# Performance work log

Measured on AMD Instinct MI355X. Metric: run time of the kernel, lower is better.

Reference implementation:

```python
import jax, jax.numpy as jnp
import numpy as np

N_NODES, N_EDGES = 50000, 200000
DN, DE, DG = 256, 256, 128

def setup_inputs() -> dict:
    key = jax.random.key(0)
    ks = jax.random.split(key, 8)
    s = lambda d: 1.0 / np.sqrt(d)
    return {
        "nodes": jax.random.normal(ks[0], (N_NODES, DN), jnp.float32),
        "edges": jax.random.normal(ks[1], (N_EDGES, DE), jnp.float32),
        "globals_": jax.random.normal(ks[2], (DG,), jnp.float32),
        "senders": jax.random.randint(ks[3], (N_EDGES,), 0, N_NODES, jnp.int32),
        "receivers": jax.random.randint(ks[4], (N_EDGES,), 0, N_NODES, jnp.int32),
        "We": jax.random.normal(ks[5], (DE + 2 * DN + DG, DE), jnp.float32) * s(DE + 2 * DN + DG),
        "be": jnp.zeros((DE,), jnp.float32),
        "Wn": jax.random.normal(ks[6], (DE + DN + DG, DN), jnp.float32) * s(DE + DN + DG),
        "bn": jnp.zeros((DN,), jnp.float32),
        "Wg": jax.random.normal(ks[7], (DE + DN + DG, DG), jnp.float32) * s(DE + DN + DG),
        "bg": jnp.zeros((DG,), jnp.float32),
    }

def reference(nodes, edges, globals_, senders, receivers, We, be, Wn, bn, Wg, bg):
    E, N = edges.shape[0], nodes.shape[0]
    # --- edge processor: phi_e([e, v_s, v_r, u]) ---
    edge_in = jnp.concatenate(
        [edges, nodes[senders], nodes[receivers],
         jnp.broadcast_to(globals_, (E, globals_.shape[0]))], axis=-1)  # [E, 896]
    new_edges = jax.nn.relu(edge_in @ We + be)  # [E, DE]
    # --- node processor: phi_v([sum_incoming_e, v, u]) ---
    agg_e = jax.ops.segment_sum(new_edges, receivers, num_segments=N)  # [N, DE]
    node_in = jnp.concatenate(
        [agg_e, nodes, jnp.broadcast_to(globals_, (N, globals_.shape[0]))], axis=-1)
    new_nodes = jax.nn.relu(node_in @ Wn + bn)  # [N, DN]
    # --- global processor: phi_u([sum_e, sum_v, u]) ---
    global_in = jnp.concatenate(
        [new_edges.sum(axis=0), new_nodes.sum(axis=0), globals_], axis=-1)
    new_globals = jax.nn.relu(global_in @ Wg + bg)  # [DG]
    return new_edges, new_nodes, new_globals
```

## Files before the change

kernel.cpp:

```cpp
#include <hip/hip_runtime.h>

#define E_CNT 200000
#define N_CNT 50000

typedef __attribute__((ext_vector_type(8))) unsigned short ushort8;
typedef __attribute__((ext_vector_type(4))) float f32x4;
typedef __bf16 bf16x8 __attribute__((ext_vector_type(8)));

static __device__ __forceinline__ unsigned short f2bf(float f) {
  unsigned int u = __builtin_bit_cast(unsigned int, f);
  u += 0x7FFFu + ((u >> 16) & 1u);
  return (unsigned short)(u >> 16);
}

typedef const __attribute__((address_space(1))) void gvoid;
typedef __attribute__((address_space(3))) void lvoid;
static __device__ __forceinline__ void gload_lds16(const void* g, void* l) {
  __builtin_amdgcn_global_load_lds((gvoid*)g, (lvoid*)l, 16, 0, 0);
}

__global__ void prep_w(const float* __restrict__ W, unsigned short* __restrict__ Bp, int KC) {
  int idx = blockIdx.x * blockDim.x + threadIdx.x;
  int total = KC * 16 * 64;
  if (idx >= total) return;
  int lane = idx & 63;
  int t = idx >> 6;
  int F = t & 15;
  int kc = t >> 4;
  int col = F * 16 + (lane & 15);
  int kb = kc * 32 + (lane >> 4) * 8;
  ushort8 v;
#pragma unroll
  for (int j = 0; j < 8; ++j) v[j] = f2bf(W[(size_t)(kb + j) * 256 + col]);
  *reinterpret_cast<ushort8*>(Bp + (size_t)idx * 8) = v;
}

template <int NSTEPS, bool EDGE>
__global__ __launch_bounds__(512, 4) void gemm_mlp(
    const float* __restrict__ in0, const float* __restrict__ nodes,
    const float* __restrict__ gl, const int* __restrict__ senders,
    const int* __restrict__ receivers, const unsigned short* __restrict__ Bp,
    const float* __restrict__ bias, float* __restrict__ out,
    float* __restrict__ agg, int M) {
  __shared__ float ldsA[2][64 * 64];

  const int tid = threadIdx.x;
  const int lane = tid & 63;
  const int wave = tid >> 6;
  const int wm = wave >> 2;
  const int wn = wave & 3;
  const int q = lane >> 4;
  const int lr = lane & 15;
  const int row0 = blockIdx.x * 64;

  int rl[2];
  const float* bp[2][4];
#pragma unroll
  for (int i = 0; i < 2; ++i) {
    rl[i] = wave * 8 + i * 4 + q;
    int e = row0 + rl[i];
    if (e > M - 1) e = M - 1;
    if (EDGE) {
      bp[i][0] = in0 + (size_t)e * 256;
      bp[i][1] = nodes + (size_t)senders[e] * 256;
      bp[i][2] = nodes + (size_t)receivers[e] * 256;
      bp[i][3] = gl;
    } else {
      bp[i][0] = in0 + (size_t)e * 256;
      bp[i][1] = nodes + (size_t)e * 256;
      bp[i][2] = gl;
      bp[i][3] = gl;
    }
  }

  f32x4 acc[2][4] = {};

#pragma unroll
  for (int i = 0; i < 2; ++i) {
    const float* src = bp[i][0] + ((lr ^ (rl[i] & 15)) << 2);
    gload_lds16(src, &ldsA[0][(wave * 8 + i * 4) * 64]);
  }
  __syncthreads();

#pragma unroll
  for (int ks = 0; ks < NSTEPS; ++ks) {
    const int buf = ks & 1;

    bf16x8 bfr[2][4];
#pragma unroll
    for (int kk = 0; kk < 2; ++kk) {
      const int kc32 = ks * 2 + kk;
#pragma unroll
      for (int fn = 0; fn < 4; ++fn) {
        const int F = wn * 4 + fn;
        bfr[kk][fn] = __builtin_bit_cast(
            bf16x8, *reinterpret_cast<const ushort8*>(
                        Bp + ((size_t)(kc32 * 16 + F) * 64 + lane) * 8));
      }
    }

    if (ks + 1 < NSTEPS) {
      const int seg = (ks + 1) >> 2;
      const int off = ((ks + 1) & 3) * 64;
#pragma unroll
      for (int i = 0; i < 2; ++i) {
        const float* src = bp[i][seg] + off + ((lr ^ (rl[i] & 15)) << 2);
        gload_lds16(src, &ldsA[buf ^ 1][(wave * 8 + i * 4) * 64]);
      }
    }
    __builtin_amdgcn_sched_barrier(0);

#pragma unroll
    for (int kk = 0; kk < 2; ++kk) {
      bf16x8 a[2];
#pragma unroll
      for (int fm = 0; fm < 2; ++fm) {
        const int r = wm * 32 + fm * 16 + lr;
        const int x = r & 15;
        const int u0 = kk * 8 + q * 2;
        f32x4 lo = *reinterpret_cast<const f32x4*>(
            &ldsA[buf][r * 64 + ((u0 ^ x) << 2)]);
        f32x4 hi = *reinterpret_cast<const f32x4*>(
            &ldsA[buf][r * 64 + (((u0 + 1) ^ x) << 2)]);
        bf16x8 av;
        av[0] = (__bf16)lo[0]; av[1] = (__bf16)lo[1];
        av[2] = (__bf16)lo[2]; av[3] = (__bf16)lo[3];
        av[4] = (__bf16)hi[0]; av[5] = (__bf16)hi[1];
        av[6] = (__bf16)hi[2]; av[7] = (__bf16)hi[3];
        a[fm] = av;
      }
#pragma unroll
      for (int fm = 0; fm < 2; ++fm)
#pragma unroll
        for (int fn = 0; fn < 4; ++fn)
          acc[fm][fn] = __builtin_amdgcn_mfma_f32_16x16x32_bf16(
              a[fm], bfr[kk][fn], acc[fm][fn], 0, 0, 0);
    }
    __syncthreads();
  }

  float bcol[4];
#pragma unroll
  for (int fn = 0; fn < 4; ++fn) bcol[fn] = bias[wn * 64 + fn * 16 + lr];
#pragma unroll
  for (int fm = 0; fm < 2; ++fm) {
    int rb = row0 + wm * 32 + fm * 16 + q * 4;
#pragma unroll
    for (int i = 0; i < 4; ++i) {
      int gr = rb + i;
      if (gr < M) {
        int rcv = 0;
        if (EDGE) rcv = receivers[gr];
#pragma unroll
        for (int fn = 0; fn < 4; ++fn) {
          int col = wn * 64 + fn * 16 + lr;
          float v = fmaxf(acc[fm][fn][i] + bcol[fn], 0.0f);
          if (EDGE) {
            __builtin_nontemporal_store(v, &out[(size_t)gr * 256 + col]);
            atomicAdd(agg + (size_t)rcv * 256 + col, v);
          } else {
            out[(size_t)gr * 256 + col] = v;
          }
        }
      }
    }
  }
}

__global__ void colsum_p1(const float* __restrict__ in, float* __restrict__ part, int rows) {
  const int c4 = threadIdx.x & 63;
  const int rg = threadIdx.x >> 6;
  f32x4 s = {0.f, 0.f, 0.f, 0.f};
  for (int r = blockIdx.x * 4 + rg; r < rows; r += 256)
    s += *reinterpret_cast<const f32x4*>(in + (size_t)r * 256 + c4 * 4);
  __shared__ f32x4 red[256];
  red[threadIdx.x] = s;
  __syncthreads();
  if (rg == 0) {
    f32x4 r = red[c4] + red[64 + c4] + red[128 + c4] + red[192 + c4];
    *reinterpret_cast<f32x4*>(part + (size_t)blockIdx.x * 256 + c4 * 4) = r;
  }
}

__global__ void colsum_p2(const float* __restrict__ part, float* __restrict__ out) {
  const int c = threadIdx.x;
  float s = 0.f;
  for (int p = 0; p < 64; ++p) s += part[(size_t)p * 256 + c];
  out[c] = s;
}

__global__ void global_mlp(const float* __restrict__ esum, const float* __restrict__ nsum,
                           const float* __restrict__ gl, const float* __restrict__ Wg,
                           const float* __restrict__ bg, float* __restrict__ out2) {
  __shared__ float red[512];
  int g = threadIdx.x & 127;
  int kg = threadIdx.x >> 7;
  float acc = 0.f;
  for (int k = kg; k < 640; k += 4) {
    float x = (k < 256) ? esum[k] : (k < 512 ? nsum[k - 256] : gl[k - 512]);
    acc += x * Wg[(size_t)k * 128 + g];
  }
  red[threadIdx.x] = acc;
  __syncthreads();
  if (kg == 0) {
    float r = red[g] + red[128 + g] + red[256 + g] + red[384 + g] + bg[g];
    out2[g] = fmaxf(r, 0.f);
  }
}

extern "C" void kernel_launch(void* const* d_in, const int* in_sizes, int n_in,
                              void* d_out, int out_size, void* d_ws, size_t ws_size,
                              hipStream_t stream) {
  const float* nodes = (const float*)d_in[0];
  const float* edges = (const float*)d_in[1];
  const float* gl = (const float*)d_in[2];
  const int* senders = (const int*)d_in[3];
  const int* receivers = (const int*)d_in[4];
  const float* We = (const float*)d_in[5];
  const float* be = (const float*)d_in[6];
  const float* Wn = (const float*)d_in[7];
  const float* bn = (const float*)d_in[8];
  const float* Wg = (const float*)d_in[9];
  const float* bg = (const float*)d_in[10];

  float* out0 = (float*)d_out;
  float* out1 = out0 + (size_t)E_CNT * 256;
  float* out2 = out1 + (size_t)N_CNT * 256;

  char* ws = (char*)d_ws;
  size_t o = 0;
  float* agg = (float*)(ws + o);                   o += (size_t)N_CNT * 256 * 4;
  float* esum = (float*)(ws + o);                  o += 1024;
  float* nsum = (float*)(ws + o);                  o += 1024;
  float* partE = (float*)(ws + o);                 o += 64 * 256 * 4;
  float* partN = (float*)(ws + o);                 o += 64 * 256 * 4;
  unsigned short* BpE = (unsigned short*)(ws + o); o += 458752;
  unsigned short* BpN = (unsigned short*)(ws + o); o += 327680;

  hipMemsetAsync(agg, 0, (size_t)N_CNT * 256 * 4, stream);

  prep_w<<<112, 256, 0, stream>>>(We, BpE, 28);
  prep_w<<<80, 256, 0, stream>>>(Wn, BpN, 20);

  gemm_mlp<14, true><<<E_CNT / 64, 512, 0, stream>>>(
      edges, nodes, gl, senders, receivers, BpE, be, out0, agg, E_CNT);

  colsum_p1<<<64, 256, 0, stream>>>(agg, partE, N_CNT);
  colsum_p2<<<1, 256, 0, stream>>>(partE, esum);

  gemm_mlp<10, false><<<(N_CNT + 63) / 64, 512, 0, stream>>>(
      agg, nodes, gl, nullptr, nullptr, BpN, bn, out1, nullptr, N_CNT);

  colsum_p1<<<64, 256, 0, stream>>>(out1, partN, N_CNT);
  colsum_p2<<<1, 256, 0, stream>>>(partN, nsum);

  global_mlp<<<1, 512, 0, stream>>>(esum, nsum, gl, Wg, bg, out2);
}
```

Before: 529.5 us.

## Pre-convert node features to bf16 and load A fragments directly into registers

Adds a pass that converts node features and globals to bf16 once, so the gathered sender/receiver rows read half the bytes. The GEMM drops the LDS double-buffered global_load_lds staging and syncthreads, loading A fragments directly from global memory into registers for each 32-wide K chunk. Column-sum partial count is doubled. This trades away the prefetch/overlap pipeline and its coalesced staging for fewer bytes and no barriers, and adds an extra conversion kernel and workspace.

```diff
diff --git a/kernel.cpp b/kernel.cpp
--- a/kernel.cpp
+++ b/kernel.cpp
@@ -11,12 +11,6 @@
   unsigned int u = __builtin_bit_cast(unsigned int, f);
   u += 0x7FFFu + ((u >> 16) & 1u);
   return (unsigned short)(u >> 16);
-}
-
-typedef const __attribute__((address_space(1))) void gvoid;
-typedef __attribute__((address_space(3))) void lvoid;
-static __device__ __forceinline__ void gload_lds16(const void* g, void* l) {
-  __builtin_amdgcn_global_load_lds((gvoid*)g, (lvoid*)l, 16, 0, 0);
 }
 
 __global__ void prep_w(const float* __restrict__ W, unsigned short* __restrict__ Bp, int KC) {
@@ -35,15 +29,28 @@
   *reinterpret_cast<ushort8*>(Bp + (size_t)idx * 8) = v;
 }
 
+__global__ void cvt_bf16(const float* __restrict__ in, unsigned short* __restrict__ outp,
+                         int n8) {
+  int i = blockIdx.x * blockDim.x + threadIdx.x;
+  if (i >= n8) return;
+  f32x4 a = *reinterpret_cast<const f32x4*>(in + (size_t)i * 8);
+  f32x4 b = *reinterpret_cast<const f32x4*>(in + (size_t)i * 8 + 4);
+  ushort8 v;
+#pragma unroll
+  for (int j = 0; j < 4; ++j) {
+    v[j] = f2bf(a[j]);
+    v[4 + j] = f2bf(b[j]);
+  }
+  *reinterpret_cast<ushort8*>(outp + (size_t)i * 8) = v;
+}
+
 template <int NSTEPS, bool EDGE>
 __global__ __launch_bounds__(512, 4) void gemm_mlp(
-    const float* __restrict__ in0, const float* __restrict__ nodes,
-    const float* __restrict__ gl, const int* __restrict__ senders,
+    const float* __restrict__ in0, const unsigned short* __restrict__ nbf,
+    const unsigned short* __restrict__ glb, const int* __restrict__ senders,
     const int* __restrict__ receivers, const unsigned short* __restrict__ Bp,
     const float* __restrict__ bias, float* __restrict__ out,
     float* __restrict__ agg, int M) {
-  __shared__ float ldsA[2][64 * 64];
-
   const int tid = threadIdx.x;
   const int lane = tid & 63;
   const int wave = tid >> 6;
@@ -51,92 +58,71 @@
   const int wn = wave & 3;
   const int q = lane >> 4;
   const int lr = lane & 15;
-  const int row0 = blockIdx.x * 64;
-
-  int rl[2];
-  const float* bp[2][4];
-#pragma unroll
-  for (int i = 0; i < 2; ++i) {
-    rl[i] = wave * 8 + i * 4 + q;
-    int e = row0 + rl[i];
-    if (e > M - 1) e = M - 1;
+  const int rowW = blockIdx.x * 64 + wm * 32;
+
+  const float* p0[2];
+  const unsigned short* p1[2];
+  const unsigned short* p2[2];
+#pragma unroll
+  for (int fm = 0; fm < 2; ++fm) {
+    int r = rowW + fm * 16 + lr;
+    if (r > M - 1) r = M - 1;
+    p0[fm] = in0 + (size_t)r * 256;
     if (EDGE) {
-      bp[i][0] = in0 + (size_t)e * 256;
-      bp[i][1] = nodes + (size_t)senders[e] * 256;
-      bp[i][2] = nodes + (size_t)receivers[e] * 256;
-      bp[i][3] = gl;
+      p1[fm] = nbf + (size_t)senders[r] * 256;
+      p2[fm] = nbf + (size_t)receivers[r] * 256;
     } else {
-      bp[i][0] = in0 + (size_t)e * 256;
-      bp[i][1] = nodes + (size_t)e * 256;
-      bp[i][2] = gl;
-      bp[i][3] = gl;
+      p1[fm] = nbf + (size_t)r * 256;
+      p2[fm] = nbf;
     }
   }
 
   f32x4 acc[2][4] = {};
 
 #pragma unroll
-  for (int i = 0; i < 2; ++i) {
-    const float* src = bp[i][0] + ((lr ^ (rl[i] & 15)) << 2);
-    gload_lds16(src, &ldsA[0][(wave * 8 + i * 4) * 64]);
-  }
-  __syncthreads();
-
-#pragma unroll
-  for (int ks = 0; ks < NSTEPS; ++ks) {
-    const int buf = ks & 1;
-
-    bf16x8 bfr[2][4];
-#pragma unroll
-    for (int kk = 0; kk < 2; ++kk) {
-      const int kc32 = ks * 2 + kk;
-#pragma unroll
-      for (int fn = 0; fn < 4; ++fn) {
-        const int F = wn * 4 + fn;
-        bfr[kk][fn] = __builtin_bit_cast(
-            bf16x8, *reinterpret_cast<const ushort8*>(
-                        Bp + ((size_t)(kc32 * 16 + F) * 64 + lane) * 8));
-      }
-    }
-
-    if (ks + 1 < NSTEPS) {
-      const int seg = (ks + 1) >> 2;
-      const int off = ((ks + 1) & 3) * 64;
-#pragma unroll
-      for (int i = 0; i < 2; ++i) {
-        const float* src = bp[i][seg] + off + ((lr ^ (rl[i] & 15)) << 2);
-        gload_lds16(src, &ldsA[buf ^ 1][(wave * 8 + i * 4) * 64]);
-      }
-    }
-    __builtin_amdgcn_sched_barrier(0);
-
-#pragma unroll
-    for (int kk = 0; kk < 2; ++kk) {
-      bf16x8 a[2];
-#pragma unroll
-      for (int fm = 0; fm < 2; ++fm) {
-        const int r = wm * 32 + fm * 16 + lr;
-        const int x = r & 15;
-        const int u0 = kk * 8 + q * 2;
-        f32x4 lo = *reinterpret_cast<const f32x4*>(
-            &ldsA[buf][r * 64 + ((u0 ^ x) << 2)]);
-        f32x4 hi = *reinterpret_cast<const f32x4*>(
-            &ldsA[buf][r * 64 + (((u0 + 1) ^ x) << 2)]);
+  for (int kc = 0; kc < NSTEPS; ++kc) {
+    const int seg = kc >> 3;
+    const int ko = (kc & 7) * 32 + q * 8;
+
+    bf16x8 a[2];
+#pragma unroll
+    for (int fm = 0; fm < 2; ++fm) {
+      if (seg == 0) {
+        f32x4 lo = *reinterpret_cast<const f32x4*>(p0[fm] + ko);
+        f32x4 hi = *reinterpret_cast<const f32x4*>(p0[fm] + ko + 4);
         bf16x8 av;
         av[0] = (__bf16)lo[0]; av[1] = (__bf16)lo[1];
         av[2] = (__bf16)lo[2]; av[3] = (__bf16)lo[3];
         av[4] = (__bf16)hi[0]; av[5] = (__bf16)hi[1];
         av[6] = (__bf16)hi[2]; av[7] = (__bf16)hi[3];
         a[fm] = av;
+      } else if (EDGE ? (seg == 1) : false) {
+        a[fm] = __builtin_bit_cast(bf16x8,
+                    *reinterpret_cast<const ushort8*>(p1[fm] + ko));
+      } else if (EDGE ? (seg == 2) : (seg == 1)) {
+        a[fm] = __builtin_bit_cast(bf16x8,
+                    *reinterpret_cast<const ushort8*>((EDGE ? p2[fm] : p1[fm]) + ko));
+      } else {
+        a[fm] = __builtin_bit_cast(bf16x8,
+                    *reinterpret_cast<const ushort8*>(glb + ko));
       }
-#pragma unroll
-      for (int fm = 0; fm < 2; ++fm)
-#pragma unroll
-        for (int fn = 0; fn < 4; ++fn)
-          acc[fm][fn] = __builtin_amdgcn_mfma_f32_16x16x32_bf16(
-              a[fm], bfr[kk][fn], acc[fm][fn], 0, 0, 0);
-    }
-    __syncthreads();
+    }
+
+    bf16x8 b[4];
+#pragma unroll
+    for (int fn = 0; fn < 4; ++fn) {
+      const int F = wn * 4 + fn;
+      b[fn] = __builtin_bit_cast(
+          bf16x8, *reinterpret_cast<const ushort8*>(
+                      Bp + ((size_t)(kc * 16 + F) * 64 + lane) * 8));
+    }
+
+#pragma unroll
+    for (int fm = 0; fm < 2; ++fm)
+#pragma unroll
+      for (int fn = 0; fn < 4; ++fn)
+        acc[fm][fn] = __builtin_amdgcn_mfma_f32_16x16x32_bf16(
+            a[fm], b[fn], acc[fm][fn], 0, 0, 0);
   }
 
   float bcol[4];
@@ -144,7 +130,7 @@
   for (int fn = 0; fn < 4; ++fn) bcol[fn] = bias[wn * 64 + fn * 16 + lr];
 #pragma unroll
   for (int fm = 0; fm < 2; ++fm) {
-    int rb = row0 + wm * 32 + fm * 16 + q * 4;
+    int rb = rowW + fm * 16 + q * 4;
 #pragma unroll
     for (int i = 0; i < 4; ++i) {
       int gr = rb + i;
@@ -167,11 +153,12 @@
   }
 }
 
+#define CS_PARTS 128
 __global__ void colsum_p1(const float* __restrict__ in, float* __restrict__ part, int rows) {
   const int c4 = threadIdx.x & 63;
   const int rg = threadIdx.x >> 6;
   f32x4 s = {0.f, 0.f, 0.f, 0.f};
-  for (int r = blockIdx.x * 4 + rg; r < rows; r += 256)
+  for (int r = blockIdx.x * 4 + rg; r < rows; r += CS_PARTS * 4)
     s += *reinterpret_cast<const f32x4*>(in + (size_t)r * 256 + c4 * 4);
   __shared__ f32x4 red[256];
   red[threadIdx.x] = s;
@@ -185,7 +172,7 @@
 __global__ void colsum_p2(const float* __restrict__ part, float* __restrict__ out) {
   const int c = threadIdx.x;
   float s = 0.f;
-  for (int p = 0; p < 64; ++p) s += part[(size_t)p * 256 + c];
+  for (int p = 0; p < CS_PARTS; ++p) s += part[(size_t)p * 256 + c];
   out[c] = s;
 }
 
@@ -232,26 +219,30 @@
   float* agg = (float*)(ws + o);                   o += (size_t)N_CNT * 256 * 4;
   float* esum = (float*)(ws + o);                  o += 1024;
   float* nsum = (float*)(ws + o);                  o += 1024;
-  float* partE = (float*)(ws + o);                 o += 64 * 256 * 4;
-  float* partN = (float*)(ws + o);                 o += 64 * 256 * 4;
+  float* partE = (float*)(ws + o);                 o += CS_PARTS * 256 * 4;
+  float* partN = (float*)(ws + o);                 o += CS_PARTS * 256 * 4;
   unsigned short* BpE = (unsigned short*)(ws + o); o += 458752;
   unsigned short* BpN = (unsigned short*)(ws + o); o += 327680;
+  unsigned short* nbf = (unsigned short*)(ws + o); o += (size_t)N_CNT * 256 * 2;
+  unsigned short* glb = (unsigned short*)(ws + o); o += 512;
 
   hipMemsetAsync(agg, 0, (size_t)N_CNT * 256 * 4, stream);
 
   prep_w<<<112, 256, 0, stream>>>(We, BpE, 28);
   prep_w<<<80, 256, 0, stream>>>(Wn, BpN, 20);
-
-  gemm_mlp<14, true><<<E_CNT / 64, 512, 0, stream>>>(
-      edges, nodes, gl, senders, receivers, BpE, be, out0, agg, E_CNT);
-
-  colsum_p1<<<64, 256, 0, stream>>>(agg, partE, N_CNT);
+  cvt_bf16<<<(N_CNT * 32 + 255) / 256, 256, 0, stream>>>(nodes, nbf, N_CNT * 32);
+  cvt_bf16<<<1, 16, 0, stream>>>(gl, glb, 16);
+
+  gemm_mlp<28, true><<<E_CNT / 64, 512, 0, stream>>>(
+      edges, nbf, glb, senders, receivers, BpE, be, out0, agg, E_CNT);
+
+  colsum_p1<<<CS_PARTS, 256, 0, stream>>>(agg, partE, N_CNT);
   colsum_p2<<<1, 256, 0, stream>>>(partE, esum);
 
-  gemm_mlp<10, false><<<(N_CNT + 63) / 64, 512, 0, stream>>>(
-      agg, nodes, gl, nullptr, nullptr, BpN, bn, out1, nullptr, N_CNT);
-
-  colsum_p1<<<64, 256, 0, stream>>>(out1, partN, N_CNT);
+  gemm_mlp<20, false><<<(N_CNT + 63) / 64, 512, 0, stream>>>(
+      agg, nbf, glb, nullptr, nullptr, BpN, bn, out1, nullptr, N_CNT);
+
+  colsum_p1<<<CS_PARTS, 256, 0, stream>>>(out1, partN, N_CNT);
   colsum_p2<<<1, 256, 0, stream>>>(partN, nsum);
 
   global_mlp<<<1, 512, 0, stream>>>(esum, nsum, gl, Wg, bg, out2);
```

Measured after the change: 635.0 us. 1.2x slower.

## Triple-buffer LDS A tiles and register-prefetch B fragments in GEMM loop

Applied to the files above, without the earlier changes.

The GEMM main loop moves from a double-buffered LDS tile to a three-deep ring. Global-to-LDS loads now run two K-steps ahead, and the next step's weight fragments are prefetched into registers one step ahead. Explicit vmcnt waits and raw s_barrier replace the per-step __syncthreads, so more memory traffic can be in flight over the MFMA work. The column-sum reduction also uses 128 partial blocks instead of 64. In exchange, each block needs 48KB of LDS and more registers, which may cut the number of resident blocks per CU.

```diff
diff --git a/kernel.cpp b/kernel.cpp
--- a/kernel.cpp
+++ b/kernel.cpp
@@ -6,6 +6,8 @@
 typedef __attribute__((ext_vector_type(8))) unsigned short ushort8;
 typedef __attribute__((ext_vector_type(4))) float f32x4;
 typedef __bf16 bf16x8 __attribute__((ext_vector_type(8)));
+
+#define WAITVM(N) asm volatile("s_waitcnt vmcnt(" #N ")" ::: "memory")
 
 static __device__ __forceinline__ unsigned short f2bf(float f) {
   unsigned int u = __builtin_bit_cast(unsigned int, f);
@@ -42,7 +44,7 @@
     const int* __restrict__ receivers, const unsigned short* __restrict__ Bp,
     const float* __restrict__ bias, float* __restrict__ out,
     float* __restrict__ agg, int M) {
-  __shared__ float ldsA[2][64 * 64];
+  __shared__ float ldsA[3][64 * 64];
 
   const int tid = threadIdx.x;
   const int lane = tid & 63;
@@ -73,40 +75,52 @@
     }
   }
 
-  f32x4 acc[2][4] = {};
-
-#pragma unroll
-  for (int i = 0; i < 2; ++i) {
-    const float* src = bp[i][0] + ((lr ^ (rl[i] & 15)) << 2);
-    gload_lds16(src, &ldsA[0][(wave * 8 + i * 4) * 64]);
-  }
-  __syncthreads();
-
-#pragma unroll
-  for (int ks = 0; ks < NSTEPS; ++ks) {
-    const int buf = ks & 1;
-
-    bf16x8 bfr[2][4];
+  auto stage = [&](int ksi, int bidx) {
+#pragma unroll
+    for (int i = 0; i < 2; ++i) {
+      const float* src = bp[i][ksi >> 2] + ((ksi & 3) << 6) + ((lr ^ (rl[i] & 15)) << 2);
+      gload_lds16(src, &ldsA[bidx][(wave * 8 + i * 4) * 64]);
+    }
+  };
+
+  auto loadB = [&](int ksi, bf16x8 (&dst)[2][4]) {
 #pragma unroll
     for (int kk = 0; kk < 2; ++kk) {
-      const int kc32 = ks * 2 + kk;
+      const int kc32 = ksi * 2 + kk;
 #pragma unroll
       for (int fn = 0; fn < 4; ++fn) {
         const int F = wn * 4 + fn;
-        bfr[kk][fn] = __builtin_bit_cast(
+        dst[kk][fn] = __builtin_bit_cast(
             bf16x8, *reinterpret_cast<const ushort8*>(
                         Bp + ((size_t)(kc32 * 16 + F) * 64 + lane) * 8));
       }
     }
-
-    if (ks + 1 < NSTEPS) {
-      const int seg = (ks + 1) >> 2;
-      const int off = ((ks + 1) & 3) * 64;
-#pragma unroll
-      for (int i = 0; i < 2; ++i) {
-        const float* src = bp[i][seg] + off + ((lr ^ (rl[i] & 15)) << 2);
-        gload_lds16(src, &ldsA[buf ^ 1][(wave * 8 + i * 4) * 64]);
-      }
+  };
+
+  f32x4 acc[2][4] = {};
+  bf16x8 bcur[2][4];
+
+  stage(0, 0);
+  stage(1, 1);
+  loadB(0, bcur);
+  WAITVM(2);
+  __builtin_amdgcn_sched_barrier(0);
+  __builtin_amdgcn_s_barrier();
+
+#pragma unroll
+  for (int t = 0; t < NSTEPS; ++t) {
+    const int buf = t % 3;
+
+    bf16x8 bnxt[2][4];
+    if (t + 1 < NSTEPS) loadB(t + 1, bnxt);
+    if (t + 2 < NSTEPS) stage(t + 2, (t + 2) % 3);
+
+    if (t + 2 < NSTEPS) {
+      WAITVM(10);
+    } else if (t + 1 < NSTEPS) {
+      WAITVM(8);
+    } else {
+      WAITVM(0);
     }
     __builtin_amdgcn_sched_barrier(0);
 
@@ -118,10 +132,9 @@
         const int r = wm * 32 + fm * 16 + lr;
         const int x = r & 15;
         const int u0 = kk * 8 + q * 2;
-        f32x4 lo = *reinterpret_cast<const f32x4*>(
-            &ldsA[buf][r * 64 + ((u0 ^ x) << 2)]);
-        f32x4 hi = *reinterpret_cast<const f32x4*>(
-            &ldsA[buf][r * 64 + (((u0 + 1) ^ x) << 2)]);
+        f32x4 lo = *reinterpret_cast<const f32x4*>(&ldsA[buf][r * 64 + ((u0 ^ x) << 2)]);
+        f32x4 hi =
+            *reinterpret_cast<const f32x4*>(&ldsA[buf][r * 64 + (((u0 + 1) ^ x) << 2)]);
         bf16x8 av;
         av[0] = (__bf16)lo[0]; av[1] = (__bf16)lo[1];
         av[2] = (__bf16)lo[2]; av[3] = (__bf16)lo[3];
@@ -134,9 +147,18 @@
 #pragma unroll
         for (int fn = 0; fn < 4; ++fn)
           acc[fm][fn] = __builtin_amdgcn_mfma_f32_16x16x32_bf16(
-              a[fm], bfr[kk][fn], acc[fm][fn], 0, 0, 0);
-    }
-    __syncthreads();
+              a[fm], bcur[kk][fn], acc[fm][fn], 0, 0, 0);
+    }
+
+    __builtin_amdgcn_sched_barrier(0);
+    __builtin_amdgcn_s_barrier();
+
+    if (t + 1 < NSTEPS) {
+#pragma unroll
+      for (int kk = 0; kk < 2; ++kk)
+#pragma unroll
+        for (int fn = 0; fn < 4; ++fn) bcur[kk][fn] = bnxt[kk][fn];
+    }
   }
 
   float bcol[4];
@@ -167,11 +189,12 @@
   }
 }
 
+#define CS_PARTS 128
 __global__ void colsum_p1(const float* __restrict__ in, float* __restrict__ part, int rows) {
   const int c4 = threadIdx.x & 63;
   const int rg = threadIdx.x >> 6;
   f32x4 s = {0.f, 0.f, 0.f, 0.f};
-  for (int r = blockIdx.x * 4 + rg; r < rows; r += 256)
+  for (int r = blockIdx.x * 4 + rg; r < rows; r += CS_PARTS * 4)
     s += *reinterpret_cast<const f32x4*>(in + (size_t)r * 256 + c4 * 4);
   __shared__ f32x4 red[256];
   red[threadIdx.x] = s;
@@ -185,7 +208,7 @@
 __global__ void colsum_p2(const float* __restrict__ part, float* __restrict__ out) {
   const int c = threadIdx.x;
   float s = 0.f;
-  for (int p = 0; p < 64; ++p) s += part[(size_t)p * 256 + c];
+  for (int p = 0; p < CS_PARTS; ++p) s += part[(size_t)p * 256 + c];
   out[c] = s;
 }
 
@@ -232,8 +255,8 @@
   float* agg = (float*)(ws + o);                   o += (size_t)N_CNT * 256 * 4;
   float* esum = (float*)(ws + o);                  o += 1024;
   float* nsum = (float*)(ws + o);                  o += 1024;
-  float* partE = (float*)(ws + o);                 o += 64 * 256 * 4;
-  float* partN = (float*)(ws + o);                 o += 64 * 256 * 4;
+  float* partE = (float*)(ws + o);                 o += CS_PARTS * 256 * 4;
+  float* partN = (float*)(ws + o);                 o += CS_PARTS * 256 * 4;
   unsigned short* BpE = (unsigned short*)(ws + o); o += 458752;
   unsigned short* BpN = (unsigned short*)(ws + o); o += 327680;
 
@@ -245,13 +268,13 @@
   gemm_mlp<14, true><<<E_CNT / 64, 512, 0, stream>>>(
       edges, nodes, gl, senders, receivers, BpE, be, out0, agg, E_CNT);
 
-  colsum_p1<<<64, 256, 0, stream>>>(agg, partE, N_CNT);
+  colsum_p1<<<CS_PARTS, 256, 0, stream>>>(agg, partE, N_CNT);
   colsum_p2<<<1, 256, 0, stream>>>(partE, esum);
 
   gemm_mlp<10, false><<<(N_CNT + 63) / 64, 512, 0, stream>>>(
       agg, nodes, gl, nullptr, nullptr, BpN, bn, out1, nullptr, N_CNT);
 
-  colsum_p1<<<64, 256, 0, stream>>>(out1, partN, N_CNT);
+  colsum_p1<<<CS_PARTS, 256, 0, stream>>>(out1, partN, N_CNT);
   colsum_p2<<<1, 256, 0, stream>>>(partN, nsum);
 
   global_mlp<<<1, 512, 0, stream>>>(esum, nsum, gl, Wg, bg, out2);
```

New measurement: 525.3 us. Within noise of the previous version (-0.8%).
